# Kernel optimization log

Measured on AMD Instinct MI355X. Metric: run time of the kernel, lower is better.

The kernel has to match this reference:

```python
import jax, jax.numpy as jnp
import numpy as np

HIDDEN = 512
SEQ = 2048
BATCH = 64


def setup_inputs() -> dict:
    key = jax.random.key(0)
    k1, k2 = jax.random.split(key)
    x = jax.random.normal(k1, (SEQ, BATCH, HIDDEN), dtype=jnp.float32)
    # weight_hh ~ uniform(0, 1) as in reset_parameters
    weight_hh = jax.random.uniform(k2, (HIDDEN,), dtype=jnp.float32)
    return {"x": x, "weight_hh": weight_hh}


def reference(x, weight_hh):
    # IndRNN (recurrent-only): h_t = relu(x_t + w_hh * h_{t-1})
    # x: [T, B, H], weight_hh: [H]
    h0 = jnp.zeros((x.shape[1], x.shape[2]), dtype=x.dtype)

    def step(h, x_t):
        h_new = jax.nn.relu(x_t + h * weight_hh)  # [B, H]
        return h_new, h_new

    _, outputs = jax.lax.scan(step, h0, x)  # outputs: [T, B, H]
    return outputs
```

## Files before the change

### kernel.cpp

```cpp
#include <hip/hip_runtime.h>


#define HIDDEN 512
#define SEQ 2048
#define BATCH 64

constexpr int NCHAIN = BATCH * HIDDEN;
constexpr int STRIDE = BATCH * HIDDEN;
constexpr int DEPTH = 32;

template <bool PF>
__device__ __forceinline__ void run_chunk(float& hv, const float wh,
                                          const float (&cur)[DEPTH],
                                          float (&nxt)[DEPTH],
                                          const float* __restrict__ xn,
                                          float* __restrict__ o) {
#pragma unroll
  for (int i = 0; i < DEPTH; ++i) {
    if (PF) nxt[i] = __builtin_nontemporal_load(xn + (long)i * STRIDE);
    hv = fmaxf(0.0f, fmaf(wh, hv, cur[i]));
    __builtin_nontemporal_store(hv, o + (long)i * STRIDE);
  }
}

__global__ __launch_bounds__(64) void indrnn_kernel(
    const float* __restrict__ x, const float* __restrict__ w,
    float* __restrict__ out) {
  const int idx = blockIdx.x * 64 + threadIdx.x;
  const float wh = w[idx & (HIDDEN - 1)];
  const float* xp = x + idx;
  float* op = out + idx;

  float bufA[DEPTH], bufB[DEPTH];
#pragma unroll
  for (int i = 0; i < DEPTH; ++i)
    bufA[i] = __builtin_nontemporal_load(xp + (long)i * STRIDE);

  float hv = 0.0f;
  int t = 0;
#pragma unroll 1
  for (; t + 2 * DEPTH < SEQ; t += 2 * DEPTH) {
    run_chunk<true>(hv, wh, bufA, bufB, xp + (long)(t + DEPTH) * STRIDE,
                    op + (long)t * STRIDE);
    run_chunk<true>(hv, wh, bufB, bufA, xp + (long)(t + 2 * DEPTH) * STRIDE,
                    op + (long)(t + DEPTH) * STRIDE);
  }
  run_chunk<true>(hv, wh, bufA, bufB, xp + (long)(t + DEPTH) * STRIDE,
                  op + (long)t * STRIDE);
  run_chunk<false>(hv, wh, bufB, bufA, nullptr,
                   op + (long)(t + DEPTH) * STRIDE);
}

extern "C" void kernel_launch(void* const* d_in, const int* in_sizes, int n_in,
                              void* d_out, int out_size, void* d_ws,
                              size_t ws_size, hipStream_t stream) {
  const float* x = (const float*)d_in[0];
  const float* w = (const float*)d_in[1];
  float* out = (float*)d_out;
  indrnn_kernel<<<NCHAIN / 64, 64, 0, stream>>>(x, w, out);
}
```

Measured before the change: 418.5 us.

## Stream inputs through an LDS ring via direct global-to-LDS loads

Replaces the register double-buffer prefetch with a 32-slot LDS ring filled by global_load_lds, issuing loads 24 steps ahead in groups of 8. Explicit vmcnt waits pace consumption, so each group waits only for its own data instead of a whole chunk. The aim is to cut VGPR pressure and keep many loads in flight per wave. The cost is an extra LDS read per element, and correctness depends on hand-computed waitcnt values, which stores also count against.

```diff
diff --git a/kernel.cpp b/kernel.cpp
--- a/kernel.cpp
+++ b/kernel.cpp
@@ -1,54 +1,91 @@
 #include <hip/hip_runtime.h>
 
 
+#define T_SEQ 2048
+#define BATCH 64
 #define HIDDEN 512
-#define SEQ 2048
-#define BATCH 64
 
+constexpr int STRIDE = BATCH * HIDDEN;
 constexpr int NCHAIN = BATCH * HIDDEN;
-constexpr int STRIDE = BATCH * HIDDEN;
-constexpr int DEPTH = 32;
+constexpr int RING = 32;
+constexpr int PD = 24;
+constexpr int GRP = 8;
 
-template <bool PF>
-__device__ __forceinline__ void run_chunk(float& hv, const float wh,
-                                          const float (&cur)[DEPTH],
-                                          float (&nxt)[DEPTH],
-                                          const float* __restrict__ xn,
-                                          float* __restrict__ o) {
+#define GLOBAL_AS __attribute__((address_space(1)))
+#define LDS_AS __attribute__((address_space(3)))
+
+constexpr unsigned vm(unsigned n) {
+  return ((n & 0x30u) << 10) | 0xF70u | (n & 0xFu);
+}
+
+template <unsigned WAITN, bool LOAD>
+__device__ __forceinline__ void group(int j0, int t0, float& hv,
+                                      const float wh,
+                                      const float* __restrict__ xp,
+                                      float* __restrict__ op,
+                                      float* ring, int lane) {
+  __builtin_amdgcn_s_waitcnt(vm(WAITN));
+  float v[GRP];
 #pragma unroll
-  for (int i = 0; i < DEPTH; ++i) {
-    if (PF) nxt[i] = __builtin_nontemporal_load(xn + (long)i * STRIDE);
-    hv = fmaxf(0.0f, fmaf(wh, hv, cur[i]));
-    __builtin_nontemporal_store(hv, o + (long)i * STRIDE);
+  for (int i = 0; i < GRP; ++i)
+    v[i] = ring[((j0 + i) & (RING - 1)) * 64 + lane];
+#pragma unroll
+  for (int i = 0; i < GRP; ++i) {
+    hv = fmaxf(0.0f, fmaf(wh, hv, v[i]));
+    __builtin_nontemporal_store(hv, op + (size_t)(t0 + i) * STRIDE);
+  }
+  if (LOAD) {
+#pragma unroll
+    for (int i = 0; i < GRP; ++i) {
+      const int t = t0 + PD + i;
+      const int slot = (j0 + PD + i) & (RING - 1);
+      __builtin_amdgcn_global_load_lds(
+          (const GLOBAL_AS void*)(xp + (size_t)t * STRIDE),
+          (LDS_AS void*)(&ring[slot * 64]), 4, 0, 0);
+    }
   }
 }
 
 __global__ __launch_bounds__(64) void indrnn_kernel(
     const float* __restrict__ x, const float* __restrict__ w,
     float* __restrict__ out) {
-  const int idx = blockIdx.x * 64 + threadIdx.x;
+  __shared__ float ring[RING * 64];
+  const int lane = threadIdx.x;
+  const int idx = blockIdx.x * 64 + lane;
   const float wh = w[idx & (HIDDEN - 1)];
   const float* xp = x + idx;
   float* op = out + idx;
 
-  float bufA[DEPTH], bufB[DEPTH];
 #pragma unroll
-  for (int i = 0; i < DEPTH; ++i)
-    bufA[i] = __builtin_nontemporal_load(xp + (long)i * STRIDE);
+  for (int j = 0; j < PD; ++j) {
+    __builtin_amdgcn_global_load_lds(
+        (const GLOBAL_AS void*)(xp + (size_t)j * STRIDE),
+        (LDS_AS void*)(&ring[j * 64]), 4, 0, 0);
+  }
 
   float hv = 0.0f;
-  int t = 0;
+
+  group<16, true>(0, 0, hv, wh, xp, op, ring, lane);
+  group<24, true>(8, 8, hv, wh, xp, op, ring, lane);
+  group<32, true>(16, 16, hv, wh, xp, op, ring, lane);
+  group<32, true>(24, 24, hv, wh, xp, op, ring, lane);
+
 #pragma unroll 1
-  for (; t + 2 * DEPTH < SEQ; t += 2 * DEPTH) {
-    run_chunk<true>(hv, wh, bufA, bufB, xp + (long)(t + DEPTH) * STRIDE,
-                    op + (long)t * STRIDE);
-    run_chunk<true>(hv, wh, bufB, bufA, xp + (long)(t + 2 * DEPTH) * STRIDE,
-                    op + (long)(t + DEPTH) * STRIDE);
+  for (int c = 1; c < T_SEQ / RING - 1; ++c) {
+    const int t0 = c * RING;
+    group<32, true>(0, t0, hv, wh, xp, op, ring, lane);
+    group<32, true>(8, t0 + 8, hv, wh, xp, op, ring, lane);
+    group<32, true>(16, t0 + 16, hv, wh, xp, op, ring, lane);
+    group<32, true>(24, t0 + 24, hv, wh, xp, op, ring, lane);
   }
-  run_chunk<true>(hv, wh, bufA, bufB, xp + (long)(t + DEPTH) * STRIDE,
-                  op + (long)t * STRIDE);
-  run_chunk<false>(hv, wh, bufB, bufA, nullptr,
-                   op + (long)(t + DEPTH) * STRIDE);
+
+  {
+    const int t0 = T_SEQ - RING;
+    group<32, true>(0, t0, hv, wh, xp, op, ring, lane);
+    group<32, false>(8, t0 + 8, hv, wh, xp, op, ring, lane);
+    group<24, false>(16, t0 + 16, hv, wh, xp, op, ring, lane);
+    group<16, false>(24, t0 + 24, hv, wh, xp, op, ring, lane);
+  }
 }
 
 extern "C" void kernel_launch(void* const* d_in, const int* in_sizes, int n_in,
```

After: 435.5 us. 1.04x slower.
